# Kernel tuning notes

Measured on AMD Instinct MI355X. Metric: run time of the kernel, lower is better.

Reference implementation:

```python
import jax, jax.numpy as jnp
import numpy as np

HID, HEADS, HD = 512, 8, 64  # hid_dim, n_heads, head_dim
NEG = -1e10


def setup_inputs() -> dict:
    key = jax.random.key(0)
    ks = jax.random.split(key, 12)
    B, S = 4, 2048
    inp = {
        'query': jax.random.normal(ks[0], (B, S, HID), jnp.float32),
        'key': jax.random.normal(ks[1], (B, S, HID), jnp.float32),
        'value': jax.random.normal(ks[2], (B, S, HID), jnp.float32),
        'mask': jnp.ones((B, 1, 1, S), jnp.int32),
    }
    sc = 1.0 / np.sqrt(HID)
    for i, n in enumerate(['Wq', 'Wk', 'Wv', 'Wo']):
        inp[n] = jax.random.uniform(ks[3 + i], (HID, HID), jnp.float32, -sc, sc)
    for i, n in enumerate(['bq', 'bk', 'bv', 'bo']):
        inp[n] = jax.random.uniform(ks[7 + i], (HID,), jnp.float32, -sc, sc)
    return inp


def reference(query, key, value, mask, Wq, Wk, Wv, Wo, bq, bk, bv, bo):
    B = query.shape[0]

    def proj(x, W, b):
        # torch Linear: x @ W.T + b; then split heads -> [B, H, S, HD]
        y = jnp.einsum('bsd,ed->bse', x, W) + b
        return y.reshape(B, -1, HEADS, HD).transpose(0, 2, 1, 3)

    Q = proj(query, Wq, bq)
    K = proj(key, Wk, bk)
    V = proj(value, Wv, bv)
    scale = jnp.sqrt(jnp.float32(HD))
    E = jnp.einsum('bhqd,bhkd->bhqk', Q, K) / scale  # [B,H,Sq,Sk]
    E = jnp.where(mask == 0, NEG, E)
    A = jax.nn.softmax(E, axis=-1)  # dropout p=0 -> identity
    out = jnp.einsum('bhqk,bhkd->bhqd', A, V)
    out = out.transpose(0, 2, 1, 3).reshape(B, -1, HID)
    return jnp.einsum('bsd,ed->bse', out, Wo) + bo
```

## Files before the change

kernel.cpp:

```cpp
#include <hip/hip_runtime.h>
#include <hip/hip_bf16.h>


typedef __bf16 v8bf __attribute__((ext_vector_type(8)));
typedef __bf16 v4bf __attribute__((ext_vector_type(4)));
typedef float  v4f  __attribute__((ext_vector_type(4)));

#define MFMA16(a, b, c) __builtin_amdgcn_mfma_f32_16x16x32_bf16((a), (b), (c), 0, 0, 0)

__device__ inline v8bf cvt8(const float* __restrict__ p) {
    const v4f f0 = *(const v4f*)p;
    const v4f f1 = *(const v4f*)(p + 4);
    v8bf r;
    r[0] = (__bf16)f0[0]; r[1] = (__bf16)f0[1]; r[2] = (__bf16)f0[2]; r[3] = (__bf16)f0[3];
    r[4] = (__bf16)f1[0]; r[5] = (__bf16)f1[1]; r[6] = (__bf16)f1[2]; r[7] = (__bf16)f1[3];
    return r;
}

__global__ __launch_bounds__(256) void cvt_w(
    const float* __restrict__ Wq, const float* __restrict__ Wk,
    const float* __restrict__ Wv, const float* __restrict__ Wo,
    __bf16* __restrict__ out)
{
    const int idx = (blockIdx.x * 256 + threadIdx.x) * 4;
    const int w = idx >> 18, off = idx & 262143;
    const float* src = (w == 0) ? Wq : (w == 1) ? Wk : (w == 2) ? Wv : Wo;
    const v4f x = *(const v4f*)(src + off);
    v4bf y;
    y[0] = (__bf16)x[0]; y[1] = (__bf16)x[1]; y[2] = (__bf16)x[2]; y[3] = (__bf16)x[3];
    *(v4bf*)(out + idx) = y;
}

__global__ __launch_bounds__(256) void qkv_gemm(
    const float* __restrict__ xq, const float* __restrict__ xk, const float* __restrict__ xv,
    const __bf16* __restrict__ Wb,
    const float* __restrict__ bq, const float* __restrict__ bk, const float* __restrict__ bv,
    __bf16* __restrict__ Qo, __bf16* __restrict__ Ko, __bf16* __restrict__ VTo)
{
    const int z = blockIdx.z;
    const float*  x    = (z == 0) ? xq : (z == 1) ? xk : xv;
    const __bf16* W    = Wb + (size_t)z * 262144;
    const float*  bias = (z == 0) ? bq : (z == 1) ? bk : bv;

    const int tid = threadIdx.x, wave = tid >> 6, lane = tid & 63;
    const int quad = lane >> 4, r = lane & 15;
    const int wm = wave >> 1, wn = wave & 1;
    const int row0 = blockIdx.x * 128, col0 = blockIdx.y * 128;

    __shared__ __align__(16) __bf16 As[8192];
    __shared__ __align__(16) __bf16 Bs[8192];

    const float*  aptr[4];
    const __bf16* bptr[4];
    int adst[4], bdst[4];
    for (int j = 0; j < 4; j++) {
        const int e = tid + 256 * j;
        const int seg = e >> 6, ln = e & 63;
        aptr[j] = x + (size_t)(row0 + (seg >> 1) * 16 + (ln & 15)) * 512
                    + (seg & 1) * 32 + (ln >> 4) * 8;
        adst[j] = e * 8;
        const int segb = wave * 4 + j;
        bptr[j] = W + (size_t)(col0 + (segb >> 1) * 16 + r) * 512
                    + (segb & 1) * 32 + quad * 8;
        bdst[j] = (segb * 64 + lane) * 8;
    }

    v4f acc[4][4] = {};
    v8bf aReg[4], bReg[4];
    for (int j = 0; j < 4; j++) {
        aReg[j] = cvt8(aptr[j]);
        bReg[j] = *(const v8bf*)bptr[j];
    }

    for (int ki = 0; ki < 8; ki++) {
        __syncthreads();
        for (int j = 0; j < 4; j++) {
            *(v8bf*)&As[adst[j]] = aReg[j];
            *(v8bf*)&Bs[bdst[j]] = bReg[j];
        }
        __syncthreads();
        if (ki < 7) {
            const int kk = (ki + 1) * 64;
            for (int j = 0; j < 4; j++) {
                aReg[j] = cvt8(aptr[j] + kk);
                bReg[j] = *(const v8bf*)(bptr[j] + kk);
            }
        }
        for (int kc = 0; kc < 2; kc++) {
            v8bf a[4], b[4];
            for (int i = 0; i < 4; i++)
                a[i] = ((const v8bf*)As)[((wm * 4 + i) * 2 + kc) * 64 + lane];
            for (int i = 0; i < 4; i++)
                b[i] = ((const v8bf*)Bs)[((wn * 4 + i) * 2 + kc) * 64 + lane];
            for (int mi = 0; mi < 4; mi++)
                for (int ni = 0; ni < 4; ni++)
                    acc[mi][ni] = MFMA16(a[mi], b[ni], acc[mi][ni]);
        }
    }

    for (int ni = 0; ni < 4; ni++) {
        const int n = col0 + wn * 64 + ni * 16 + r;
        const float bv_ = bias[n];
        const int hh = n >> 6, hd = n & 63;
        for (int mi = 0; mi < 4; mi++) {
            const int mbase = row0 + wm * 64 + mi * 16 + quad * 4;
            const int bb = mbase >> 11, s0 = mbase & 2047;
            if (z == 2) {
                v4bf pk;
                for (int i = 0; i < 4; i++)
                    pk[i] = (__bf16)(acc[mi][ni][i] + bv_);
                *(v4bf*)&VTo[((size_t)((bb * 8 + hh) * 64 + hd)) * 2048 + s0] = pk;
            } else {
                __bf16* dst = (z == 0) ? Qo : Ko;
                for (int i = 0; i < 4; i++)
                    dst[((size_t)((bb * 8 + hh) * 2048 + s0 + i)) * 64 + hd] =
                        (__bf16)(acc[mi][ni][i] + bv_);
            }
        }
    }
}

__global__ __launch_bounds__(256) void attn(
    const __bf16* __restrict__ Q, const __bf16* __restrict__ K,
    const __bf16* __restrict__ VT, const int* __restrict__ mask,
    __bf16* __restrict__ AO)
{
    const int bh = blockIdx.y, b = bh >> 3, h = bh & 7;
    const int tid = threadIdx.x, wave = tid >> 6, lane = tid & 63;
    const int quad = lane >> 4, r = lane & 15;
    const int q0 = blockIdx.x * 64 + wave * 16;

    const __bf16* Qb = Q  + (size_t)bh * 2048 * 64;
    const __bf16* Kb = K  + (size_t)bh * 2048 * 64;
    const __bf16* Vb = VT + (size_t)bh * 64 * 2048;
    const int*    mb = mask + (size_t)b * 2048;

    __shared__ __align__(16) __bf16 Kls[4096];
    __shared__ __align__(16) __bf16 Vls[4096];
    __shared__ __align__(16) __bf16 Pls[4][16][72];
    __shared__ __bf16 biasLS[2048];

    for (int i = tid; i < 2048; i += 256)
        biasLS[i] = (mb[i] != 0) ? (__bf16)0.f : (__bf16)(-1e10f);

    const int e1 = tid, e2 = tid + 256;
    int seg, l, t_, h_, rr, qd;
    seg = e1 >> 6; l = e1 & 63; t_ = seg >> 1; h_ = seg & 1; rr = l & 15; qd = l >> 4;
    const __bf16* kg1 = Kb + (size_t)(16 * t_ + rr) * 64   + h_ * 32 + qd * 8;
    const __bf16* vg1 = Vb + (size_t)(16 * t_ + rr) * 2048 + h_ * 32 + qd * 8;
    seg = e2 >> 6; l = e2 & 63; t_ = seg >> 1; h_ = seg & 1; rr = l & 15; qd = l >> 4;
    const __bf16* kg2 = Kb + (size_t)(16 * t_ + rr) * 64   + h_ * 32 + qd * 8;
    const __bf16* vg2 = Vb + (size_t)(16 * t_ + rr) * 2048 + h_ * 32 + qd * 8;

    v8bf qf0 = *(const v8bf*)(Qb + (size_t)(q0 + r) * 64 +      quad * 8);
    v8bf qf1 = *(const v8bf*)(Qb + (size_t)(q0 + r) * 64 + 32 + quad * 8);

    float ssum = 0.f;
    v4f o[4] = {};

    v8bf ks1 = *(const v8bf*)kg1, ks2 = *(const v8bf*)kg2;
    v8bf vs1 = *(const v8bf*)vg1, vs2 = *(const v8bf*)vg2;

    for (int t = 0; t < 32; t++) {
        __syncthreads();
        ((v8bf*)Kls)[e1] = ks1; ((v8bf*)Kls)[e2] = ks2;
        ((v8bf*)Vls)[e1] = vs1; ((v8bf*)Vls)[e2] = vs2;
        __syncthreads();
        if (t < 31) {
            const int k0n = (t + 1) * 64;
            ks1 = *(const v8bf*)(kg1 + (size_t)k0n * 64);
            ks2 = *(const v8bf*)(kg2 + (size_t)k0n * 64);
            vs1 = *(const v8bf*)(vg1 + k0n);
            vs2 = *(const v8bf*)(vg2 + k0n);
        }
        const int k0 = t * 64;

        v4f sa[4] = {};
        for (int tt = 0; tt < 4; tt++) {
            v8bf kf0 = ((const v8bf*)Kls)[(tt * 2 + 0) * 64 + lane];
            v8bf kf1 = ((const v8bf*)Kls)[(tt * 2 + 1) * 64 + lane];
            sa[tt] = MFMA16(kf0, qf0, sa[tt]);
            sa[tt] = MFMA16(kf1, qf1, sa[tt]);
        }

        for (int tt = 0; tt < 4; tt++) {
            const v4bf bl = *(const v4bf*)&biasLS[k0 + tt * 16 + quad * 4];
            v4bf pk;
            for (int i = 0; i < 4; i++) {
                const float p = __expf(fmaf(sa[tt][i], 0.125f, (float)bl[i]));
                ssum += p;
                pk[i] = (__bf16)p;
            }
            *(v4bf*)&Pls[wave][r][tt * 16 + quad * 4] = pk;
        }
        asm volatile("s_waitcnt lgkmcnt(0)" ::: "memory");
        v8bf pa0 = *(const v8bf*)&Pls[wave][r][     quad * 8];
        v8bf pa1 = *(const v8bf*)&Pls[wave][r][32 + quad * 8];

        for (int t2 = 0; t2 < 4; t2++) {
            v8bf vf0 = ((const v8bf*)Vls)[(t2 * 2 + 0) * 64 + lane];
            v8bf vf1 = ((const v8bf*)Vls)[(t2 * 2 + 1) * 64 + lane];
            o[t2] = MFMA16(pa0, vf0, o[t2]);
            o[t2] = MFMA16(pa1, vf1, o[t2]);
        }
    }

    ssum += __shfl_xor(ssum, 16);
    ssum += __shfl_xor(ssum, 32);
    float lr[4];
    for (int i = 0; i < 4; i++) lr[i] = __shfl(ssum, quad * 4 + i);

    for (int t2 = 0; t2 < 4; t2++) {
        const int hd = t2 * 16 + r;
        for (int i = 0; i < 4; i++) {
            const int s = q0 + quad * 4 + i;
            AO[((size_t)b * 2048 + s) * 512 + h * 64 + hd] = (__bf16)(o[t2][i] / lr[i]);
        }
    }
}

__global__ __launch_bounds__(256) void out_gemm(
    const __bf16* __restrict__ Ai, const __bf16* __restrict__ W,
    const float* __restrict__ bias, float* __restrict__ y)
{
    const int tid = threadIdx.x, wave = tid >> 6, lane = tid & 63;
    const int quad = lane >> 4, r = lane & 15;
    const int wm = wave >> 1, wn = wave & 1;
    const int row0 = blockIdx.x * 128, col0 = blockIdx.y * 128;

    __shared__ __align__(16) __bf16 As[8192];
    __shared__ __align__(16) __bf16 Bs[8192];

    const __bf16* aptr[4];
    const __bf16* bptr[4];
    int dst_[4];
    for (int j = 0; j < 4; j++) {
        const int segb = wave * 4 + j;
        aptr[j] = Ai + (size_t)(row0 + (segb >> 1) * 16 + r) * 512 + (segb & 1) * 32 + quad * 8;
        bptr[j] = W  + (size_t)(col0 + (segb >> 1) * 16 + r) * 512 + (segb & 1) * 32 + quad * 8;
        dst_[j] = (segb * 64 + lane) * 8;
    }

    v4f acc[4][4] = {};
    v8bf aReg[4], bReg[4];
    for (int j = 0; j < 4; j++) {
        aReg[j] = *(const v8bf*)aptr[j];
        bReg[j] = *(const v8bf*)bptr[j];
    }

    for (int ki = 0; ki < 8; ki++) {
        __syncthreads();
        for (int j = 0; j < 4; j++) {
            *(v8bf*)&As[dst_[j]] = aReg[j];
            *(v8bf*)&Bs[dst_[j]] = bReg[j];
        }
        __syncthreads();
        if (ki < 7) {
            const int kk = (ki + 1) * 64;
            for (int j = 0; j < 4; j++) {
                aReg[j] = *(const v8bf*)(aptr[j] + kk);
                bReg[j] = *(const v8bf*)(bptr[j] + kk);
            }
        }
        for (int kc = 0; kc < 2; kc++) {
            v8bf a[4], b[4];
            for (int i = 0; i < 4; i++)
                a[i] = ((const v8bf*)As)[((wm * 4 + i) * 2 + kc) * 64 + lane];
            for (int i = 0; i < 4; i++)
                b[i] = ((const v8bf*)Bs)[((wn * 4 + i) * 2 + kc) * 64 + lane];
            for (int mi = 0; mi < 4; mi++)
                for (int ni = 0; ni < 4; ni++)
                    acc[mi][ni] = MFMA16(a[mi], b[ni], acc[mi][ni]);
        }
    }

    for (int ni = 0; ni < 4; ni++) {
        const int n = col0 + wn * 64 + ni * 16 + r;
        const float bv_ = bias[n];
        for (int mi = 0; mi < 4; mi++) {
            const int mbase = row0 + wm * 64 + mi * 16 + quad * 4;
            for (int i = 0; i < 4; i++)
                y[(size_t)(mbase + i) * 512 + n] = acc[mi][ni][i] + bv_;
        }
    }
}

extern "C" void kernel_launch(void* const* d_in, const int* in_sizes, int n_in,
                              void* d_out, int out_size, void* d_ws, size_t ws_size,
                              hipStream_t stream)
{
    const float* q    = (const float*)d_in[0];
    const float* k    = (const float*)d_in[1];
    const float* v    = (const float*)d_in[2];
    const int*   mask = (const int*)d_in[3];
    const float* Wq   = (const float*)d_in[4];
    const float* Wk   = (const float*)d_in[5];
    const float* Wv   = (const float*)d_in[6];
    const float* Wo   = (const float*)d_in[7];
    const float* bq   = (const float*)d_in[8];
    const float* bk   = (const float*)d_in[9];
    const float* bv   = (const float*)d_in[10];
    const float* bo   = (const float*)d_in[11];

    __bf16* ws  = (__bf16*)d_ws;
    __bf16* Qw  = ws;
    __bf16* Kw  = ws + 4194304;
    __bf16* VTw = ws + 8388608;
    __bf16* AOw = ws + 12582912;
    __bf16* Wb  = ws + 16777216;

    cvt_w<<<dim3(1024), 256, 0, stream>>>(Wq, Wk, Wv, Wo, Wb);
    qkv_gemm<<<dim3(64, 4, 3), 256, 0, stream>>>(q, k, v, Wb, bq, bk, bv, Qw, Kw, VTw);
    attn<<<dim3(32, 32), 256, 0, stream>>>(Qw, Kw, VTw, mask, AOw);
    out_gemm<<<dim3(64, 4), 256, 0, stream>>>(AOw, Wb + 786432, bo, (float*)d_out);
}
```

Baseline: 238.4 us.

## Load K/V fragments directly from global, drop LDS staging and block barriers

The attention kernel stops staging K and V tiles through shared memory. Each wave now reads its MFMA fragments straight from global memory, which removes the two __syncthreads per tile. Other changes: the block index is remapped so neighbouring blocks share heads for L2 locality, the softmax uses exp2 with a prescaled constant and a float bias, the row sum is computed with an extra MFMA against a ones vector, and launch bounds request 4 blocks per CU. The trade-off is redundant global/L2 traffic, since the four waves each load the same K/V, in exchange for fewer barriers and less LDS use, which allows higher occupancy.

```diff
diff --git a/kernel.cpp b/kernel.cpp
--- a/kernel.cpp
+++ b/kernel.cpp
@@ -120,101 +120,89 @@
     }
 }
 
-__global__ __launch_bounds__(256) void attn(
+__global__ __launch_bounds__(256, 4) void attn(
     const __bf16* __restrict__ Q, const __bf16* __restrict__ K,
     const __bf16* __restrict__ VT, const int* __restrict__ mask,
     __bf16* __restrict__ AO)
 {
-    const int bh = blockIdx.y, b = bh >> 3, h = bh & 7;
+    const int id = blockIdx.y * 32 + blockIdx.x;
+    const int x8 = id & 7, j = (id >> 3) & 3, qb = id >> 5;
+    const int bh = x8 * 4 + j;
+    const int b = bh >> 3, h = bh & 7;
     const int tid = threadIdx.x, wave = tid >> 6, lane = tid & 63;
     const int quad = lane >> 4, r = lane & 15;
-    const int q0 = blockIdx.x * 64 + wave * 16;
+    const int q0 = qb * 64 + wave * 16;
 
     const __bf16* Qb = Q  + (size_t)bh * 2048 * 64;
     const __bf16* Kb = K  + (size_t)bh * 2048 * 64;
     const __bf16* Vb = VT + (size_t)bh * 64 * 2048;
     const int*    mb = mask + (size_t)b * 2048;
 
-    __shared__ __align__(16) __bf16 Kls[4096];
-    __shared__ __align__(16) __bf16 Vls[4096];
+    __shared__ __align__(16) float  biasF[2048];
     __shared__ __align__(16) __bf16 Pls[4][16][72];
-    __shared__ __bf16 biasLS[2048];
 
     for (int i = tid; i < 2048; i += 256)
-        biasLS[i] = (mb[i] != 0) ? (__bf16)0.f : (__bf16)(-1e10f);
-
-    const int e1 = tid, e2 = tid + 256;
-    int seg, l, t_, h_, rr, qd;
-    seg = e1 >> 6; l = e1 & 63; t_ = seg >> 1; h_ = seg & 1; rr = l & 15; qd = l >> 4;
-    const __bf16* kg1 = Kb + (size_t)(16 * t_ + rr) * 64   + h_ * 32 + qd * 8;
-    const __bf16* vg1 = Vb + (size_t)(16 * t_ + rr) * 2048 + h_ * 32 + qd * 8;
-    seg = e2 >> 6; l = e2 & 63; t_ = seg >> 1; h_ = seg & 1; rr = l & 15; qd = l >> 4;
-    const __bf16* kg2 = Kb + (size_t)(16 * t_ + rr) * 64   + h_ * 32 + qd * 8;
-    const __bf16* vg2 = Vb + (size_t)(16 * t_ + rr) * 2048 + h_ * 32 + qd * 8;
-
-    v8bf qf0 = *(const v8bf*)(Qb + (size_t)(q0 + r) * 64 +      quad * 8);
-    v8bf qf1 = *(const v8bf*)(Qb + (size_t)(q0 + r) * 64 + 32 + quad * 8);
-
-    float ssum = 0.f;
+        biasF[i] = (mb[i] != 0) ? 0.f : -1.0e10f;
+    __syncthreads();
+
+    const v8bf qf0 = *(const v8bf*)(Qb + (size_t)(q0 + r) * 64 +      quad * 8);
+    const v8bf qf1 = *(const v8bf*)(Qb + (size_t)(q0 + r) * 64 + 32 + quad * 8);
+
+    v8bf ones;
+    for (int i = 0; i < 8; i++) ones[i] = (__bf16)1.0f;
+
     v4f o[4] = {};
-
-    v8bf ks1 = *(const v8bf*)kg1, ks2 = *(const v8bf*)kg2;
-    v8bf vs1 = *(const v8bf*)vg1, vs2 = *(const v8bf*)vg2;
+    v4f osum = {};
+
+    const float SC = 0.18033688f;
 
     for (int t = 0; t < 32; t++) {
-        __syncthreads();
-        ((v8bf*)Kls)[e1] = ks1; ((v8bf*)Kls)[e2] = ks2;
-        ((v8bf*)Vls)[e1] = vs1; ((v8bf*)Vls)[e2] = vs2;
-        __syncthreads();
-        if (t < 31) {
-            const int k0n = (t + 1) * 64;
-            ks1 = *(const v8bf*)(kg1 + (size_t)k0n * 64);
-            ks2 = *(const v8bf*)(kg2 + (size_t)k0n * 64);
-            vs1 = *(const v8bf*)(vg1 + k0n);
-            vs2 = *(const v8bf*)(vg2 + k0n);
-        }
         const int k0 = t * 64;
+
+        v8bf vf[4][2];
+        for (int t2 = 0; t2 < 4; t2++)
+            for (int kc = 0; kc < 2; kc++)
+                vf[t2][kc] = *(const v8bf*)(Vb + (size_t)(t2 * 16 + r) * 2048
+                                            + k0 + kc * 32 + quad * 8);
 
         v4f sa[4] = {};
         for (int tt = 0; tt < 4; tt++) {
-            v8bf kf0 = ((const v8bf*)Kls)[(tt * 2 + 0) * 64 + lane];
-            v8bf kf1 = ((const v8bf*)Kls)[(tt * 2 + 1) * 64 + lane];
+            const size_t krow = (size_t)(k0 + tt * 16 + r) * 64;
+            const v8bf kf0 = *(const v8bf*)(Kb + krow +      quad * 8);
+            const v8bf kf1 = *(const v8bf*)(Kb + krow + 32 + quad * 8);
             sa[tt] = MFMA16(kf0, qf0, sa[tt]);
             sa[tt] = MFMA16(kf1, qf1, sa[tt]);
         }
 
         for (int tt = 0; tt < 4; tt++) {
-            const v4bf bl = *(const v4bf*)&biasLS[k0 + tt * 16 + quad * 4];
+            const v4f bl = *(const v4f*)&biasF[k0 + tt * 16 + quad * 4];
             v4bf pk;
             for (int i = 0; i < 4; i++) {
-                const float p = __expf(fmaf(sa[tt][i], 0.125f, (float)bl[i]));
-                ssum += p;
+                const float p = __builtin_amdgcn_exp2f(fmaf(sa[tt][i], SC, bl[i]));
                 pk[i] = (__bf16)p;
             }
             *(v4bf*)&Pls[wave][r][tt * 16 + quad * 4] = pk;
         }
         asm volatile("s_waitcnt lgkmcnt(0)" ::: "memory");
-        v8bf pa0 = *(const v8bf*)&Pls[wave][r][     quad * 8];
-        v8bf pa1 = *(const v8bf*)&Pls[wave][r][32 + quad * 8];
+        const v8bf pa0 = *(const v8bf*)&Pls[wave][r][     quad * 8];
+        const v8bf pa1 = *(const v8bf*)&Pls[wave][r][32 + quad * 8];
+
+        osum = MFMA16(pa0, ones, osum);
+        osum = MFMA16(pa1, ones, osum);
 
         for (int t2 = 0; t2 < 4; t2++) {
-            v8bf vf0 = ((const v8bf*)Vls)[(t2 * 2 + 0) * 64 + lane];
-            v8bf vf1 = ((const v8bf*)Vls)[(t2 * 2 + 1) * 64 + lane];
-            o[t2] = MFMA16(pa0, vf0, o[t2]);
-            o[t2] = MFMA16(pa1, vf1, o[t2]);
-        }
-    }
-
-    ssum += __shfl_xor(ssum, 16);
-    ssum += __shfl_xor(ssum, 32);
-    float lr[4];
-    for (int i = 0; i < 4; i++) lr[i] = __shfl(ssum, quad * 4 + i);
-
+            o[t2] = MFMA16(pa0, vf[t2][0], o[t2]);
+            o[t2] = MFMA16(pa1, vf[t2][1], o[t2]);
+        }
+    }
+
+    float inv[4];
+    for (int i = 0; i < 4; i++) inv[i] = 1.0f / osum[i];
     for (int t2 = 0; t2 < 4; t2++) {
         const int hd = t2 * 16 + r;
         for (int i = 0; i < 4; i++) {
             const int s = q0 + quad * 4 + i;
-            AO[((size_t)b * 2048 + s) * 512 + h * 64 + hd] = (__bf16)(o[t2][i] / lr[i]);
+            AO[((size_t)b * 2048 + s) * 512 + h * 64 + hd] = (__bf16)(o[t2][i] * inv[i]);
         }
     }
 }
```

New measurement: 396.9 us. +66.5%, slower.

## Process two query tiles per wave in attention, sum rows via MFMA

Applied to the files above, without the earlier changes.

Each wave now handles 32 query rows instead of 16, so each K/V tile staged in LDS feeds twice as many MFMAs and the grid is halved. The row-sum of probabilities is computed with an MFMA against a vector of ones, matching the bf16-rounded P used for the output, in place of scalar adds and shuffles. Exp is done with exp2 and a prescaled constant, the mask bias is kept in fp32, and blocks are remapped so neighbouring blocks share batch-head data in cache. The cost is more registers per thread, capped by launch bounds of 2 blocks, and fewer blocks in flight.

```diff
diff --git a/kernel.cpp b/kernel.cpp
--- a/kernel.cpp
+++ b/kernel.cpp
@@ -120,15 +120,18 @@
     }
 }
 
-__global__ __launch_bounds__(256) void attn(
+__global__ __launch_bounds__(256, 2) void attn(
     const __bf16* __restrict__ Q, const __bf16* __restrict__ K,
     const __bf16* __restrict__ VT, const int* __restrict__ mask,
     __bf16* __restrict__ AO)
 {
-    const int bh = blockIdx.y, b = bh >> 3, h = bh & 7;
+    const int id = blockIdx.y * 16 + blockIdx.x;
+    const int x8 = id & 7, j = (id >> 3) & 3, qb = id >> 5;
+    const int bh = x8 * 4 + j;
+    const int b = bh >> 3, h = bh & 7;
     const int tid = threadIdx.x, wave = tid >> 6, lane = tid & 63;
     const int quad = lane >> 4, r = lane & 15;
-    const int q0 = blockIdx.x * 64 + wave * 16;
+    const int q0 = qb * 128 + wave * 32;
 
     const __bf16* Qb = Q  + (size_t)bh * 2048 * 64;
     const __bf16* Kb = K  + (size_t)bh * 2048 * 64;
@@ -137,11 +140,11 @@
 
     __shared__ __align__(16) __bf16 Kls[4096];
     __shared__ __align__(16) __bf16 Vls[4096];
-    __shared__ __align__(16) __bf16 Pls[4][16][72];
-    __shared__ __bf16 biasLS[2048];
+    __shared__ __align__(16) float  biasF[2048];
+    __shared__ __align__(16) __bf16 Pls[4][2][16][72];
 
     for (int i = tid; i < 2048; i += 256)
-        biasLS[i] = (mb[i] != 0) ? (__bf16)0.f : (__bf16)(-1e10f);
+        biasF[i] = (mb[i] != 0) ? 0.f : -1.0e10f;
 
     const int e1 = tid, e2 = tid + 256;
     int seg, l, t_, h_, rr, qd;
@@ -152,11 +155,19 @@
     const __bf16* kg2 = Kb + (size_t)(16 * t_ + rr) * 64   + h_ * 32 + qd * 8;
     const __bf16* vg2 = Vb + (size_t)(16 * t_ + rr) * 2048 + h_ * 32 + qd * 8;
 
-    v8bf qf0 = *(const v8bf*)(Qb + (size_t)(q0 + r) * 64 +      quad * 8);
-    v8bf qf1 = *(const v8bf*)(Qb + (size_t)(q0 + r) * 64 + 32 + quad * 8);
-
-    float ssum = 0.f;
-    v4f o[4] = {};
+    v8bf qf[2][2];
+    for (int g = 0; g < 2; g++) {
+        qf[g][0] = *(const v8bf*)(Qb + (size_t)(q0 + g * 16 + r) * 64 +      quad * 8);
+        qf[g][1] = *(const v8bf*)(Qb + (size_t)(q0 + g * 16 + r) * 64 + 32 + quad * 8);
+    }
+
+    v8bf ones;
+    for (int i = 0; i < 8; i++) ones[i] = (__bf16)1.0f;
+
+    v4f o[2][4] = {};
+    v4f osum[2] = {};
+
+    const float SC = 0.18033688f;
 
     v8bf ks1 = *(const v8bf*)kg1, ks2 = *(const v8bf*)kg2;
     v8bf vs1 = *(const v8bf*)vg1, vs2 = *(const v8bf*)vg2;
@@ -175,46 +186,59 @@
         }
         const int k0 = t * 64;
 
-        v4f sa[4] = {};
+        v4f sa[2][4] = {};
         for (int tt = 0; tt < 4; tt++) {
-            v8bf kf0 = ((const v8bf*)Kls)[(tt * 2 + 0) * 64 + lane];
-            v8bf kf1 = ((const v8bf*)Kls)[(tt * 2 + 1) * 64 + lane];
-            sa[tt] = MFMA16(kf0, qf0, sa[tt]);
-            sa[tt] = MFMA16(kf1, qf1, sa[tt]);
+            const v8bf kf0 = ((const v8bf*)Kls)[(tt * 2 + 0) * 64 + lane];
+            const v8bf kf1 = ((const v8bf*)Kls)[(tt * 2 + 1) * 64 + lane];
+            sa[0][tt] = MFMA16(kf0, qf[0][0], sa[0][tt]);
+            sa[0][tt] = MFMA16(kf1, qf[0][1], sa[0][tt]);
+            sa[1][tt] = MFMA16(kf0, qf[1][0], sa[1][tt]);
+            sa[1][tt] = MFMA16(kf1, qf[1][1], sa[1][tt]);
         }
 
         for (int tt = 0; tt < 4; tt++) {
-            const v4bf bl = *(const v4bf*)&biasLS[k0 + tt * 16 + quad * 4];
-            v4bf pk;
+            const v4f bl = *(const v4f*)&biasF[k0 + tt * 16 + quad * 4];
+            for (int g = 0; g < 2; g++) {
+                v4bf pk;
+                for (int i = 0; i < 4; i++) {
+                    const float p = __builtin_amdgcn_exp2f(fmaf(sa[g][tt][i], SC, bl[i]));
+                    pk[i] = (__bf16)p;
+                }
+                *(v4bf*)&Pls[wave][g][r][tt * 16 + quad * 4] = pk;
+            }
+        }
+        asm volatile("s_waitcnt lgkmcnt(0)" ::: "memory");
+        v8bf pa[2][2];
+        for (int g = 0; g < 2; g++) {
+            pa[g][0] = *(const v8bf*)&Pls[wave][g][r][     quad * 8];
+            pa[g][1] = *(const v8bf*)&Pls[wave][g][r][32 + quad * 8];
+        }
+
+        osum[0] = MFMA16(pa[0][0], ones, osum[0]);
+        osum[0] = MFMA16(pa[0][1], ones, osum[0]);
+        osum[1] = MFMA16(pa[1][0], ones, osum[1]);
+        osum[1] = MFMA16(pa[1][1], ones, osum[1]);
+
+        for (int t2 = 0; t2 < 4; t2++) {
+            const v8bf vf0 = ((const v8bf*)Vls)[(t2 * 2 + 0) * 64 + lane];
+            const v8bf vf1 = ((const v8bf*)Vls)[(t2 * 2 + 1) * 64 + lane];
+            o[0][t2] = MFMA16(pa[0][0], vf0, o[0][t2]);
+            o[0][t2] = MFMA16(pa[0][1], vf1, o[0][t2]);
+            o[1][t2] = MFMA16(pa[1][0], vf0, o[1][t2]);
+            o[1][t2] = MFMA16(pa[1][1], vf1, o[1][t2]);
+        }
+    }
+
+    for (int g = 0; g < 2; g++) {
+        float inv[4];
+        for (int i = 0; i < 4; i++) inv[i] = 1.0f / osum[g][i];
+        for (int t2 = 0; t2 < 4; t2++) {
+            const int hd = t2 * 16 + r;
             for (int i = 0; i < 4; i++) {
-                const float p = __expf(fmaf(sa[tt][i], 0.125f, (float)bl[i]));
-                ssum += p;
-                pk[i] = (__bf16)p;
-            }
-            *(v4bf*)&Pls[wave][r][tt * 16 + quad * 4] = pk;
-        }
-        asm volatile("s_waitcnt lgkmcnt(0)" ::: "memory");
-        v8bf pa0 = *(const v8bf*)&Pls[wave][r][     quad * 8];
-        v8bf pa1 = *(const v8bf*)&Pls[wave][r][32 + quad * 8];
-
-        for (int t2 = 0; t2 < 4; t2++) {
-            v8bf vf0 = ((const v8bf*)Vls)[(t2 * 2 + 0) * 64 + lane];
-            v8bf vf1 = ((const v8bf*)Vls)[(t2 * 2 + 1) * 64 + lane];
-            o[t2] = MFMA16(pa0, vf0, o[t2]);
-            o[t2] = MFMA16(pa1, vf1, o[t2]);
-        }
-    }
-
-    ssum += __shfl_xor(ssum, 16);
-    ssum += __shfl_xor(ssum, 32);
-    float lr[4];
-    for (int i = 0; i < 4; i++) lr[i] = __shfl(ssum, quad * 4 + i);
-
-    for (int t2 = 0; t2 < 4; t2++) {
-        const int hd = t2 * 16 + r;
-        for (int i = 0; i < 4; i++) {
-            const int s = q0 + quad * 4 + i;
-            AO[((size_t)b * 2048 + s) * 512 + h * 64 + hd] = (__bf16)(o[t2][i] / lr[i]);
+                const int s = q0 + g * 16 + quad * 4 + i;
+                AO[((size_t)b * 2048 + s) * 512 + h * 64 + hd] =
+                    (__bf16)(o[g][t2][i] * inv[i]);
+            }
         }
     }
 }
@@ -311,6 +335,6 @@
 
     cvt_w<<<dim3(1024), 256, 0, stream>>>(Wq, Wk, Wv, Wo, Wb);
     qkv_gemm<<<dim3(64, 4, 3), 256, 0, stream>>>(q, k, v, Wb, bq, bk, bv, Qw, Kw, VTw);
-    attn<<<dim3(32, 32), 256, 0, stream>>>(Qw, Kw, VTw, mask, AOw);
+    attn<<<dim3(16, 32), 256, 0, stream>>>(Qw, Kw, VTw, mask, AOw);
     out_gemm<<<dim3(64, 4), 256, 0, stream>>>(AOw, Wb + 786432, bo, (float*)d_out);
 }
```

Measured after the change: 220.1 us. 1.08x faster.
